# Kernel tuning notes

Hardware: AMD Instinct MI355X
Metric: run time of the kernel (lower is better)

## Reference

```python
import jax, jax.numpy as jnp
import numpy as np

B, N, H = 16, 128, 256


def setup_inputs() -> dict:
    key = jax.random.key(0)
    ks = jax.random.split(key, 7)
    s = 1.0 / np.sqrt(H)
    return {
        "inputs": jax.random.normal(ks[0], (B, N, H), dtype=jnp.float32),
        "bin_features": jax.random.normal(ks[1], (B, N, N, H), dtype=jnp.float32),
        "W_atom": jax.random.normal(ks[2], (H, H), dtype=jnp.float32) * s,
        "W_bin": jax.random.normal(ks[3], (H, H), dtype=jnp.float32) * s,
        "b_bin": jax.random.normal(ks[4], (H,), dtype=jnp.float32) * s,
        "w_score": jax.random.normal(ks[5], (H, 1), dtype=jnp.float32) * s,
        "b_score": jax.random.normal(ks[6], (1,), dtype=jnp.float32) * s,
    }


def reference(inputs, bin_features, W_atom, W_bin, b_bin, w_score, b_score):
    # atom_pair[b,i,j,h] = inputs[b,i,h] + inputs[b,j,h]
    atom_pair = inputs[:, :, None, :] + inputs[:, None, :, :]  # [B,N,N,H]
    # Linear(no bias) on atom_pair + Linear(bias) on bin_features, then ReLU.
    # Exploit linearity: (x_i + x_j) @ W = (x@W)_i + (x@W)_j to avoid an extra N^2 GEMM.
    xw = jnp.einsum('bnh,hk->bnk', inputs, W_atom)  # [B,N,H]
    att_hidden = jax.nn.relu(
        xw[:, :, None, :] + xw[:, None, :, :]
        + jnp.einsum('bijh,hk->bijk', bin_features, W_bin) + b_bin
    )  # [B,N,N,H]
    att_score = jnp.einsum('bijh,ho->bijo', att_hidden, w_score) + b_score  # [B,N,N,1]
    # att_context = att_score * inputs.unsqueeze(2); sum over j (dim 2)
    att_context = (att_score * inputs[:, :, None, :]).sum(axis=2)  # [B,N,H]
    return att_context, atom_pair
```

## Files before the change

### kernel.cpp

```cpp
#include <hip/hip_runtime.h>
#include <hip/hip_bf16.h>

#define H 256
#define NN 128
#define BB 16

typedef __attribute__((ext_vector_type(8))) __bf16 bf16x8;
typedef __attribute__((ext_vector_type(8))) short  s16x8;
typedef __attribute__((ext_vector_type(4))) short  s16x4;
typedef __attribute__((ext_vector_type(4))) float  f32x4;

__device__ __forceinline__ unsigned short f2b(float f) {
    unsigned u = __float_as_uint(f);
    u = (u + 0x7fffu + ((u >> 16) & 1u)) >> 16;
    return (unsigned short)u;
}

__global__ void k_prep_w(const float* __restrict__ Wb, unsigned short* __restrict__ WT) {
    int k = blockIdx.x;
    int h = threadIdx.x;
    WT[k * H + h] = f2b(Wb[h * H + k]);
}

__global__ void k_xw(const float* __restrict__ inp, const float* __restrict__ Wa,
                     float* __restrict__ xw) {
    __shared__ float rows[8][H];
    int r0 = blockIdx.x * 8;
    int t = threadIdx.x;
    #pragma unroll
    for (int r = 0; r < 8; ++r) rows[r][t] = inp[(r0 + r) * H + t];
    __syncthreads();
    float acc[8] = {0.f, 0.f, 0.f, 0.f, 0.f, 0.f, 0.f, 0.f};
    for (int h = 0; h < H; ++h) {
        float wv = Wa[h * H + t];
        #pragma unroll
        for (int r = 0; r < 8; ++r) acc[r] += rows[r][h] * wv;
    }
    #pragma unroll
    for (int r = 0; r < 8; ++r) xw[(r0 + r) * H + t] = acc[r];
}

__global__ __launch_bounds__(256) void k_main(
        const float* __restrict__ inp, const float* __restrict__ binf,
        const float* __restrict__ xw, const unsigned short* __restrict__ WT,
        const float* __restrict__ b_bin, const float* __restrict__ w_score,
        const float* __restrict__ b_score,
        float* __restrict__ out_ctx, float* __restrict__ out_pair) {
    __shared__ unsigned short Ab[64 * 260];
    __shared__ float base_l[H];
    __shared__ float wsc_l[H];
    __shared__ float ini_l[H];
    __shared__ float wred[4];
    __shared__ float Sp;

    int bid = blockIdx.x;
    int jt = bid & 1;
    int i  = (bid >> 1) & 127;
    int b  = bid >> 8;
    int t  = threadIdx.x;
    int bi = b * 128 + i;
    int jbase = jt * 64;

    base_l[t] = xw[bi * H + t] + b_bin[t];
    wsc_l[t]  = w_score[t];
    ini_l[t]  = inp[bi * H + t];

    const float4* bp = (const float4*)(binf + ((long)bi * 128 + jbase) * H);
    #pragma unroll
    for (int it = 0; it < 16; ++it) {
        int idx = it * 256 + t;
        float4 v = bp[idx];
        int row = idx >> 6;
        int col = (idx & 63) * 4;
        ushort4 w;
        w.x = f2b(v.x); w.y = f2b(v.y); w.z = f2b(v.z); w.w = f2b(v.w);
        *(ushort4*)&Ab[row * 260 + col] = w;
    }
    __syncthreads();

    int wave = t >> 6, lane = t & 63, q = lane >> 4, m16 = lane & 15;
    int colbase = wave * 64;

    f32x4 acc[4][4];
    #pragma unroll
    for (int rt = 0; rt < 4; ++rt)
        #pragma unroll
        for (int ct = 0; ct < 4; ++ct)
            acc[rt][ct] = (f32x4){0.f, 0.f, 0.f, 0.f};

    #pragma unroll
    for (int ks = 0; ks < 8; ++ks) {
        bf16x8 afr[4];
        #pragma unroll
        for (int rt = 0; rt < 4; ++rt) {
            const unsigned short* p = &Ab[(rt * 16 + m16) * 260 + ks * 32 + q * 8];
            s16x4 a0 = *(const s16x4*)p;
            s16x4 a1 = *(const s16x4*)(p + 4);
            s16x8 sv = __builtin_shufflevector(a0, a1, 0, 1, 2, 3, 4, 5, 6, 7);
            afr[rt] = __builtin_bit_cast(bf16x8, sv);
        }
        #pragma unroll
        for (int ct = 0; ct < 4; ++ct) {
            const unsigned short* wp = WT + (colbase + ct * 16 + m16) * H + ks * 32 + q * 8;
            bf16x8 bfr = __builtin_bit_cast(bf16x8, *(const s16x8*)wp);
            #pragma unroll
            for (int rt = 0; rt < 4; ++rt)
                acc[rt][ct] = __builtin_amdgcn_mfma_f32_16x16x32_bf16(afr[rt], bfr, acc[rt][ct], 0, 0, 0);
        }
    }

    float sacc = 0.f;
    const float* xwp = xw + ((long)b * 128 + jbase) * H;
    #pragma unroll
    for (int rt = 0; rt < 4; ++rt) {
        #pragma unroll
        for (int ct = 0; ct < 4; ++ct) {
            int k = colbase + ct * 16 + m16;
            float bs = base_l[k], wv = wsc_l[k];
            #pragma unroll
            for (int r = 0; r < 4; ++r) {
                int jl = rt * 16 + q * 4 + r;
                float hv = acc[rt][ct][r] + bs + xwp[jl * H + k];
                hv = fmaxf(hv, 0.f);
                sacc += hv * wv;
            }
        }
    }
    #pragma unroll
    for (int m = 1; m < 64; m <<= 1) sacc += __shfl_xor(sacc, m, 64);
    if (lane == 0) wred[wave] = sacc;
    __syncthreads();
    if (t == 0) Sp = wred[0] + wred[1] + wred[2] + wred[3] + 64.0f * b_score[0];
    __syncthreads();

    float iv = ini_l[t];
    float S  = Sp;
    const float* inb  = inp + ((long)b * 128 + jbase) * H;
    float* pout = out_pair + (((long)bi) * 128 + jbase) * H;
    #pragma unroll 4
    for (int j = 0; j < 64; ++j) {
        float v = inb[j * H + t];
        pout[j * H + t] = iv + v;
    }
    atomicAdd(&out_ctx[bi * H + t], iv * S);
}

extern "C" void kernel_launch(void* const* d_in, const int* in_sizes, int n_in,
                              void* d_out, int out_size, void* d_ws, size_t ws_size,
                              hipStream_t stream) {
    const float* inp     = (const float*)d_in[0];
    const float* binf    = (const float*)d_in[1];
    const float* W_atom  = (const float*)d_in[2];
    const float* W_bin   = (const float*)d_in[3];
    const float* b_bin   = (const float*)d_in[4];
    const float* w_score = (const float*)d_in[5];
    const float* b_score = (const float*)d_in[6];

    float* out_ctx  = (float*)d_out;
    float* out_pair = (float*)d_out + BB * NN * H;

    float* xw = (float*)d_ws;
    unsigned short* WT = (unsigned short*)((char*)d_ws + (size_t)BB * NN * H * 4);

    hipMemsetAsync(d_out, 0, (size_t)BB * NN * H * sizeof(float), stream);
    k_prep_w<<<H, H, 0, stream>>>(W_bin, WT);
    k_xw<<<BB * NN / 8, H, 0, stream>>>(inp, W_atom, xw);
    k_main<<<BB * NN * 2, 256, 0, stream>>>(inp, binf, xw, WT, b_bin, w_score,
                                            b_score, out_ctx, out_pair);
}
```

Baseline: 537.2 us.

## Process full j-range per block with double-buffered bin_features pipeline

Each block now handles one (b,i) row across all 128 j in four 32-row chunks. Register prefetch of the next chunk overlaps with bf16 conversion and MFMA through a double-buffered LDS tile. Because a single block owns each output row, the memset and atomicAdd are dropped, and the atom_pair writes use vectorized nontemporal stores interleaved per chunk. The cost is more registers (launch_bounds 4), half as many blocks, and an extra barrier per chunk.

After: 783.3 us. +45.8%, slower.

```diff
diff --git a/kernel.cpp b/kernel.cpp
--- a/kernel.cpp
+++ b/kernel.cpp
@@ -1,5 +1,4 @@
 #include <hip/hip_runtime.h>
-#include <hip/hip_bf16.h>
 
 #define H 256
 #define NN 128
@@ -9,11 +8,18 @@
 typedef __attribute__((ext_vector_type(8))) short  s16x8;
 typedef __attribute__((ext_vector_type(4))) short  s16x4;
 typedef __attribute__((ext_vector_type(4))) float  f32x4;
+typedef __attribute__((ext_vector_type(4))) unsigned short u16x4;
 
 __device__ __forceinline__ unsigned short f2b(float f) {
     unsigned u = __float_as_uint(f);
     u = (u + 0x7fffu + ((u >> 16) & 1u)) >> 16;
     return (unsigned short)u;
+}
+
+__device__ __forceinline__ u16x4 cvt4(f32x4 f) {
+    u16x4 w;
+    w[0] = f2b(f[0]); w[1] = f2b(f[1]); w[2] = f2b(f[2]); w[3] = f2b(f[3]);
+    return w;
 }
 
 __global__ void k_prep_w(const float* __restrict__ Wb, unsigned short* __restrict__ WT) {
@@ -40,109 +46,129 @@
     for (int r = 0; r < 8; ++r) xw[(r0 + r) * H + t] = acc[r];
 }
 
-__global__ __launch_bounds__(256) void k_main(
+__global__ __launch_bounds__(256, 4) void k_main(
         const float* __restrict__ inp, const float* __restrict__ binf,
         const float* __restrict__ xw, const unsigned short* __restrict__ WT,
         const float* __restrict__ b_bin, const float* __restrict__ w_score,
         const float* __restrict__ b_score,
         float* __restrict__ out_ctx, float* __restrict__ out_pair) {
-    __shared__ unsigned short Ab[64 * 260];
-    __shared__ float base_l[H];
-    __shared__ float wsc_l[H];
-    __shared__ float ini_l[H];
+    __shared__ __align__(16) unsigned short Ab[2][32 * 260];
+    __shared__ __align__(16) float base_l[H];
+    __shared__ __align__(16) float wsc_l[H];
+    __shared__ __align__(16) float ini_l[H];
     __shared__ float wred[4];
-    __shared__ float Sp;
 
-    int bid = blockIdx.x;
-    int jt = bid & 1;
-    int i  = (bid >> 1) & 127;
-    int b  = bid >> 8;
+    int bi = blockIdx.x;
     int t  = threadIdx.x;
-    int bi = b * 128 + i;
-    int jbase = jt * 64;
+    int b  = bi >> 7;
 
     base_l[t] = xw[bi * H + t] + b_bin[t];
     wsc_l[t]  = w_score[t];
     ini_l[t]  = inp[bi * H + t];
 
-    const float4* bp = (const float4*)(binf + ((long)bi * 128 + jbase) * H);
+    const f32x4* bp = (const f32x4*)(binf + (size_t)bi * NN * H);
+
+    f32x4 v[8];
+
     #pragma unroll
-    for (int it = 0; it < 16; ++it) {
+    for (int it = 0; it < 8; ++it) v[it] = bp[it * 256 + t];
+    #pragma unroll
+    for (int it = 0; it < 8; ++it) {
         int idx = it * 256 + t;
-        float4 v = bp[idx];
-        int row = idx >> 6;
-        int col = (idx & 63) * 4;
-        ushort4 w;
-        w.x = f2b(v.x); w.y = f2b(v.y); w.z = f2b(v.z); w.w = f2b(v.w);
-        *(ushort4*)&Ab[row * 260 + col] = w;
+        int row = idx >> 6, col = (idx & 63) * 4;
+        *(u16x4*)&Ab[0][row * 260 + col] = cvt4(v[it]);
     }
+    #pragma unroll
+    for (int it = 0; it < 8; ++it) v[it] = bp[2048 + it * 256 + t];
     __syncthreads();
 
     int wave = t >> 6, lane = t & 63, q = lane >> 4, m16 = lane & 15;
     int colbase = wave * 64;
+    float sacc = 0.f;
+    float iv_s = ini_l[t];
+    int cur = 0;
 
-    f32x4 acc[4][4];
-    #pragma unroll
-    for (int rt = 0; rt < 4; ++rt)
+    for (int jt = 0; jt < 4; ++jt) {
+        if (jt < 3) {
+            #pragma unroll
+            for (int it = 0; it < 8; ++it) {
+                int idx = it * 256 + t;
+                int row = idx >> 6, col = (idx & 63) * 4;
+                *(u16x4*)&Ab[cur ^ 1][row * 260 + col] = cvt4(v[it]);
+            }
+        }
+        if (jt < 2) {
+            #pragma unroll
+            for (int it = 0; it < 8; ++it) v[it] = bp[(size_t)(jt + 2) * 2048 + it * 256 + t];
+        }
+
+        f32x4 acc[2][4];
         #pragma unroll
-        for (int ct = 0; ct < 4; ++ct)
-            acc[rt][ct] = (f32x4){0.f, 0.f, 0.f, 0.f};
+        for (int rt = 0; rt < 2; ++rt)
+            #pragma unroll
+            for (int ct = 0; ct < 4; ++ct)
+                acc[rt][ct] = (f32x4){0.f, 0.f, 0.f, 0.f};
 
-    #pragma unroll
-    for (int ks = 0; ks < 8; ++ks) {
-        bf16x8 afr[4];
+        const unsigned short* Abc = Ab[cur];
         #pragma unroll
-        for (int rt = 0; rt < 4; ++rt) {
-            const unsigned short* p = &Ab[(rt * 16 + m16) * 260 + ks * 32 + q * 8];
-            s16x4 a0 = *(const s16x4*)p;
-            s16x4 a1 = *(const s16x4*)(p + 4);
-            s16x8 sv = __builtin_shufflevector(a0, a1, 0, 1, 2, 3, 4, 5, 6, 7);
-            afr[rt] = __builtin_bit_cast(bf16x8, sv);
+        for (int ks = 0; ks < 8; ++ks) {
+            bf16x8 afr[2];
+            #pragma unroll
+            for (int rt = 0; rt < 2; ++rt) {
+                const unsigned short* p = &Abc[(rt * 16 + m16) * 260 + ks * 32 + q * 8];
+                s16x4 a0 = *(const s16x4*)p;
+                s16x4 a1 = *(const s16x4*)(p + 4);
+                s16x8 sv = __builtin_shufflevector(a0, a1, 0, 1, 2, 3, 4, 5, 6, 7);
+                afr[rt] = __builtin_bit_cast(bf16x8, sv);
+            }
+            #pragma unroll
+            for (int ct = 0; ct < 4; ++ct) {
+                const unsigned short* wp = WT + (colbase + ct * 16 + m16) * H + ks * 32 + q * 8;
+                bf16x8 bfr = __builtin_bit_cast(bf16x8, *(const s16x8*)wp);
+                #pragma unroll
+                for (int rt = 0; rt < 2; ++rt)
+                    acc[rt][ct] = __builtin_amdgcn_mfma_f32_16x16x32_bf16(afr[rt], bfr, acc[rt][ct], 0, 0, 0);
+            }
         }
+
+        const float* xwp = xw + ((size_t)(b * NN) + jt * 32) * H;
         #pragma unroll
-        for (int ct = 0; ct < 4; ++ct) {
-            const unsigned short* wp = WT + (colbase + ct * 16 + m16) * H + ks * 32 + q * 8;
-            bf16x8 bfr = __builtin_bit_cast(bf16x8, *(const s16x8*)wp);
+        for (int rt = 0; rt < 2; ++rt) {
             #pragma unroll
-            for (int rt = 0; rt < 4; ++rt)
-                acc[rt][ct] = __builtin_amdgcn_mfma_f32_16x16x32_bf16(afr[rt], bfr, acc[rt][ct], 0, 0, 0);
+            for (int ct = 0; ct < 4; ++ct) {
+                int k = colbase + ct * 16 + m16;
+                float bs = base_l[k], wv = wsc_l[k];
+                #pragma unroll
+                for (int r = 0; r < 4; ++r) {
+                    int jl = rt * 16 + q * 4 + r;
+                    float hv = acc[rt][ct][r] + bs + xwp[jl * H + k];
+                    sacc += fmaxf(hv, 0.f) * wv;
+                }
+            }
         }
+
+        const f32x4* inb4  = (const f32x4*)(inp + ((size_t)(b * NN) + jt * 32) * H);
+        f32x4*       pout4 = (f32x4*)(out_pair + ((size_t)bi * NN + jt * 32) * H);
+        const f32x4* ini4  = (const f32x4*)ini_l;
+        #pragma unroll
+        for (int it = 0; it < 8; ++it) {
+            int idx = it * 256 + t;
+            f32x4 pv = inb4[idx];
+            pv += ini4[idx & 63];
+            __builtin_nontemporal_store(pv, &pout4[idx]);
+        }
+
+        __syncthreads();
+        cur ^= 1;
     }
 
-    float sacc = 0.f;
-    const float* xwp = xw + ((long)b * 128 + jbase) * H;
-    #pragma unroll
-    for (int rt = 0; rt < 4; ++rt) {
-        #pragma unroll
-        for (int ct = 0; ct < 4; ++ct) {
-            int k = colbase + ct * 16 + m16;
-            float bs = base_l[k], wv = wsc_l[k];
-            #pragma unroll
-            for (int r = 0; r < 4; ++r) {
-                int jl = rt * 16 + q * 4 + r;
-                float hv = acc[rt][ct][r] + bs + xwp[jl * H + k];
-                hv = fmaxf(hv, 0.f);
-                sacc += hv * wv;
-            }
-        }
-    }
     #pragma unroll
     for (int m = 1; m < 64; m <<= 1) sacc += __shfl_xor(sacc, m, 64);
     if (lane == 0) wred[wave] = sacc;
     __syncthreads();
-    if (t == 0) Sp = wred[0] + wred[1] + wred[2] + wred[3] + 64.0f * b_score[0];
+    if (t == 0) wred[0] = wred[0] + wred[1] + wred[2] + wred[3] + 128.0f * b_score[0];
     __syncthreads();
-
-    float iv = ini_l[t];
-    float S  = Sp;
-    const float* inb  = inp + ((long)b * 128 + jbase) * H;
-    float* pout = out_pair + (((long)bi) * 128 + jbase) * H;
-    #pragma unroll 4
-    for (int j = 0; j < 64; ++j) {
-        float v = inb[j * H + t];
-        pout[j * H + t] = iv + v;
-    }
-    atomicAdd(&out_ctx[bi * H + t], iv * S);
+    out_ctx[bi * H + t] = iv_s * wred[0];
 }
 
 extern "C" void kernel_launch(void* const* d_in, const int* in_sizes, int n_in,
@@ -162,9 +188,8 @@
     float* xw = (float*)d_ws;
     unsigned short* WT = (unsigned short*)((char*)d_ws + (size_t)BB * NN * H * 4);
 
-    hipMemsetAsync(d_out, 0, (size_t)BB * NN * H * sizeof(float), stream);
     k_prep_w<<<H, H, 0, stream>>>(W_bin, WT);
     k_xw<<<BB * NN / 8, H, 0, stream>>>(inp, W_atom, xw);
-    k_main<<<BB * NN * 2, 256, 0, stream>>>(inp, binf, xw, WT, b_bin, w_score,
-                                            b_score, out_ctx, out_pair);
+    k_main<<<BB * NN, 256, 0, stream>>>(inp, binf, xw, WT, b_bin, w_score,
+                                        b_score, out_ctx, out_pair);
 }
```
